# Optimization experiments

Measured on AMD Instinct MI355X. Metric: run time of the kernel, lower is better.

## Reference

```python
import jax, jax.numpy as jnp
import numpy as np

N = 50000      # nodes
E = 800000     # edges
G = 512        # graphs
IN = 544; HID = 64; H = 4; OUT = 2
EPS = 1e-5

def setup_inputs():
    key = jax.random.key(0)
    ks = jax.random.split(key, 16)
    x = jax.random.normal(ks[0], (N, IN), jnp.float32)
    edge_index = jax.random.randint(ks[1], (2, E), 0, N, jnp.int64)
    batch = jnp.sort(jax.random.randint(ks[2], (N,), 0, G, jnp.int64))
    s = lambda k, shp, fan: jax.random.normal(k, shp, jnp.float32) / np.sqrt(fan)
    return {
        'x': x, 'edge_index': edge_index, 'batch': batch,
        'ln_g': jnp.ones((32,), jnp.float32), 'ln_b': jnp.zeros((32,), jnp.float32),
        'bn1_g': jnp.ones((512,), jnp.float32), 'bn1_b': jnp.zeros((512,), jnp.float32),
        'Wc': s(ks[3], (16, 512), 512), 'bc': jnp.zeros((16,), jnp.float32),
        'bn2_g': jnp.ones((48,), jnp.float32), 'bn2_b': jnp.zeros((48,), jnp.float32),
        'Wp': s(ks[4], (HID, 48), 48), 'bp': jnp.zeros((HID,), jnp.float32),
        'Wg': s(ks[5], (H * HID, HID), HID),
        'att_src': s(ks[6], (H, HID), HID), 'att_dst': s(ks[7], (H, HID), HID),
        'bg': jnp.zeros((H * HID,), jnp.float32),
        'bn3_g': jnp.ones((H * HID,), jnp.float32), 'bn3_b': jnp.zeros((H * HID,), jnp.float32),
        'W1': s(ks[8], (HID, H * HID), H * HID), 'b1': jnp.zeros((HID,), jnp.float32),
        'W2': s(ks[9], (OUT, HID), HID), 'b2': jnp.zeros((OUT,), jnp.float32),
    }

def _batchnorm(x, g, b):
    mu = jnp.mean(x, axis=0)
    var = jnp.var(x, axis=0)
    return (x - mu) * jax.lax.rsqrt(var + EPS) * g + b

def _forward(x, ln_g, ln_b, bn1_g, bn1_b, Wc, bc, bn2_g, bn2_b, Wp, bp,
             Wg, att_src, att_dst, bg, bn3_g, bn3_b, W1, b1, W2, b2,
             edge_index, batch):
    # feature split + norms
    x_cnn = _batchnorm(x[:, :512], bn1_g, bn1_b)
    f = x[:, 512:]
    mu = jnp.mean(f, axis=-1, keepdims=True)
    var = jnp.var(f, axis=-1, keepdims=True)
    f = (f - mu) * jax.lax.rsqrt(var + EPS) * ln_g + ln_b
    x_cnn = x_cnn @ Wc.T + bc                      # [N,16]
    z = jnp.concatenate([x_cnn, f], axis=1)        # [N,48]
    z = _batchnorm(z, bn2_g, bn2_b)
    z = jax.nn.relu(z @ Wp.T + bp)                 # [N,HID] (dropout=eval identity)
    # GATConv (concat=True, negative_slope=0.2)
    h = (z @ Wg.T).reshape(N, H, HID)              # [N,H,C]
    a_src = jnp.sum(h * att_src, axis=-1)          # [N,H]
    a_dst = jnp.sum(h * att_dst, axis=-1)          # [N,H]
    src, dst = edge_index[0], edge_index[1]
    e = jax.nn.leaky_relu(a_src[src] + a_dst[dst], 0.2)   # [E,H]
    m = jax.ops.segment_max(e, dst, num_segments=N)
    m = jnp.where(jnp.isfinite(m), m, 0.0)
    ex = jnp.exp(e - m[dst])
    s = jax.ops.segment_sum(ex, dst, num_segments=N)
    alpha = ex / jnp.maximum(s, 1e-16)[dst]               # [E,H]
    out = jax.ops.segment_sum(alpha[:, :, None] * h[src], dst, num_segments=N)
    out = out.reshape(N, H * HID) + bg
    # BatchNorm + ELU + mean pool + MLP head
    out = jax.nn.elu(_batchnorm(out, bn3_g, bn3_b))
    cnt = jax.ops.segment_sum(jnp.ones((N,), out.dtype), batch, num_segments=G)
    pooled = jax.ops.segment_sum(out, batch, num_segments=G) / jnp.maximum(cnt, 1.0)[:, None]
    hmlp = jax.nn.relu(pooled @ W1.T + b1)
    return hmlp @ W2.T + b2                        # [G,OUT]

def reference(x, edge_index, batch, ln_g, ln_b, bn1_g, bn1_b, Wc, bc, bn2_g, bn2_b,
              Wp, bp, Wg, att_src, att_dst, bg, bn3_g, bn3_b, W1, b1, W2, b2):
    return _forward(x, ln_g, ln_b, bn1_g, bn1_b, Wc, bc, bn2_g, bn2_b, Wp, bp,
                    Wg, att_src, att_dst, bg, bn3_g, bn3_b, W1, b1, W2, b2,
                    edge_index, batch)
```

## Files before the change

### kernel.cpp

```cpp
#include <hip/hip_runtime.h>

static constexpr int N_   = 50000;
static constexpr int E_   = 800000;
static constexpr int G_   = 512;
static constexpr int IN_  = 544;
static constexpr float EPS_ = 1e-5f;

static constexpr int BN1C = 32;
static constexpr int BN3C = 16;
static constexpr int BN2C = 8;
static constexpr size_t OFF_BN1C   = 0;
static constexpr size_t OFF_BN2C   = 131072;
static constexpr size_t OFF_BN3C   = 134144;
static constexpr size_t OFF_COUNT  = 166912;
static constexpr size_t OFF_CUR    = 366912;
static constexpr size_t ZERO_BYTES = 566912;
static constexpr size_t OFF_OFFS   = 566912;
static constexpr size_t OFF_WC2    = 766912;
static constexpr size_t OFF_C2     = 799680;
static constexpr size_t OFF_WP2    = 799744;
static constexpr size_t OFF_CP     = 812032;
static constexpr size_t OFF_WGT    = 812288;
static constexpr size_t OFF_PART   = 877824;
static constexpr size_t OFF_ASRC   = 878080;
static constexpr size_t OFF_ADST   = 1678080;
static constexpr size_t OFF_SRCS   = 2478080;
static constexpr size_t OFF_Z      = 5678080;
static constexpr size_t OFF_H      = 15278080;
static constexpr size_t OFF_OUTP   = 40878080;

#define DEV static __device__ __forceinline__

DEV float lrelu(float v) { return v > 0.f ? v : 0.2f * v; }
DEV unsigned short f2bf(float f) {
    unsigned u = __float_as_uint(f);
    return (unsigned short)((u + 0x7fffu + ((u >> 16) & 1u)) >> 16);
}

__global__ __launch_bounds__(256) void k_bn1_hist(
        const float* __restrict__ x, float* __restrict__ bn1c,
        const int* __restrict__ ei, int* __restrict__ count) {
    __shared__ float4 ta[256];
    __shared__ float4 tb[256];
    int t = threadIdx.x;
    int cq = t & 127, rsub = t >> 7;
    int c4 = cq << 2;
    float4 a = make_float4(0.f, 0.f, 0.f, 0.f);
    float4 b = make_float4(0.f, 0.f, 0.f, 0.f);
    for (int r = blockIdx.x * 2 + rsub; r < N_; r += gridDim.x * 2) {
        float4 v = *(const float4*)(x + (size_t)r * IN_ + c4);
        a.x += v.x; a.y += v.y; a.z += v.z; a.w += v.w;
        b.x += v.x * v.x; b.y += v.y * v.y; b.z += v.z * v.z; b.w += v.w * v.w;
    }
    ta[t] = a; tb[t] = b;
    __syncthreads();
    if (t < 128) {
        float4 sa = ta[t], sb = tb[t];
        float4 xa = ta[128 + t], xb = tb[128 + t];
        sa.x += xa.x; sa.y += xa.y; sa.z += xa.z; sa.w += xa.w;
        sb.x += xb.x; sb.y += xb.y; sb.z += xb.z; sb.w += xb.w;
        float* dst = bn1c + (size_t)(blockIdx.x & (BN1C - 1)) * 1024;
        int c = t << 2;
        atomicAdd(&dst[c + 0], sa.x); atomicAdd(&dst[c + 1], sa.y);
        atomicAdd(&dst[c + 2], sa.z); atomicAdd(&dst[c + 3], sa.w);
        atomicAdd(&dst[512 + c + 0], sb.x); atomicAdd(&dst[512 + c + 1], sb.y);
        atomicAdd(&dst[512 + c + 2], sb.z); atomicAdd(&dst[512 + c + 3], sb.w);
    }
    for (int k = blockIdx.x * 256 + t; k < E_; k += gridDim.x * 256)
        atomicAdd(&count[ei[E_ + k]], 1);
}

__global__ __launch_bounds__(512) void k_fold1(
        const float* __restrict__ bn1c,
        const float* __restrict__ g, const float* __restrict__ b,
        const float* __restrict__ Wc, const float* __restrict__ bc,
        float* __restrict__ Wc2t, float* __restrict__ c2) {
    __shared__ float c2s[16];
    int j = threadIdx.x;
    if (j < 16) c2s[j] = 0.f;
    float sum = 0.f, sq = 0.f;
    for (int c = 0; c < BN1C; c++) {
        sum += bn1c[c * 1024 + j];
        sq  += bn1c[c * 1024 + 512 + j];
    }
    float mu  = sum / (float)N_;
    float var = sq / (float)N_ - mu * mu;
    float s   = g[j] * rsqrtf(var + EPS_);
    float tj  = b[j] - mu * s;
    __syncthreads();
    for (int i = 0; i < 16; i++) {
        float wv = Wc[i * 512 + j];
        Wc2t[i * 512 + j] = wv * s;
        float p = tj * wv;
        for (int m = 1; m < 64; m <<= 1) p += __shfl_xor(p, m);
        if ((j & 63) == 0) atomicAdd(&c2s[i], p);
    }
    __syncthreads();
    if (j < 16) c2[j] = c2s[j] + bc[j];
}

static constexpr int WSTRIDE = 516;
__global__ __launch_bounds__(512) void k_z(
        const float* __restrict__ x, const float* __restrict__ Wc2tg,
        const float* __restrict__ c2g, const float* __restrict__ lng,
        const float* __restrict__ lnb, float* __restrict__ z,
        float* __restrict__ bn2c) {
    __shared__ float wc2[16 * WSTRIDE];
    __shared__ float c2s[16];
    __shared__ float bsum[48];
    __shared__ float bsq[48];
    int t = threadIdx.x;
    for (int q = t; q < 8192; q += 512) {
        int row = q >> 9, col = q & 511;
        wc2[row * WSTRIDE + col] = Wc2tg[q];
    }
    if (t < 16) c2s[t] = c2g[t];
    if (t < 48) { bsum[t] = 0.f; bsq[t] = 0.f; }
    __syncthreads();
    int pr = t >> 3, i = t & 7;
    int n0 = blockIdx.x * 128 + pr * 2;
    int n1 = n0 + 1;
    bool v0 = n0 < N_, v1 = n1 < N_;
    const float4* xr0 = (const float4*)(x + (size_t)(v0 ? n0 : N_ - 1) * IN_);
    const float4* xr1 = (const float4*)(x + (size_t)(v1 ? n1 : N_ - 1) * IN_);
    const float4* w0 = (const float4*)(wc2 + i * WSTRIDE);
    const float4* w1 = (const float4*)(wc2 + (i + 8) * WSTRIDE);
    float a00 = c2s[i], a01 = c2s[i + 8];
    float a10 = a00, a11 = a01;
    for (int u = 0; u < 128; u++) {
        float4 xa = xr0[u], xb = xr1[u];
        float4 p = w0[u], q4 = w1[u];
        a00 += xa.x * p.x + xa.y * p.y + xa.z * p.z + xa.w * p.w;
        a01 += xa.x * q4.x + xa.y * q4.y + xa.z * q4.z + xa.w * q4.w;
        a10 += xb.x * p.x + xb.y * p.y + xb.z * p.z + xb.w * p.w;
        a11 += xb.x * q4.x + xb.y * q4.y + xb.z * q4.z + xb.w * q4.w;
    }
    float va[4], vb[4];
    float sm0 = 0.f, sq0 = 0.f, sm1 = 0.f, sq1 = 0.f;
#pragma unroll
    for (int jj = 0; jj < 4; jj++) {
        va[jj] = x[(size_t)(v0 ? n0 : N_ - 1) * IN_ + 512 + i + 8 * jj];
        vb[jj] = x[(size_t)(v1 ? n1 : N_ - 1) * IN_ + 512 + i + 8 * jj];
        sm0 += va[jj]; sq0 += va[jj] * va[jj];
        sm1 += vb[jj]; sq1 += vb[jj] * vb[jj];
    }
    for (int m = 1; m < 8; m <<= 1) {
        sm0 += __shfl_xor(sm0, m); sq0 += __shfl_xor(sq0, m);
        sm1 += __shfl_xor(sm1, m); sq1 += __shfl_xor(sq1, m);
    }
    float mu0 = sm0 * (1.f / 32.f), rs0 = rsqrtf(sq0 * (1.f / 32.f) - mu0 * mu0 + EPS_);
    float mu1 = sm1 * (1.f / 32.f), rs1 = rsqrtf(sq1 * (1.f / 32.f) - mu1 * mu1 + EPS_);
    float outa[6], outb[6];
    outa[0] = a00; outa[1] = a01; outb[0] = a10; outb[1] = a11;
#pragma unroll
    for (int jj = 0; jj < 4; jj++) {
        int c = i + 8 * jj;
        float gg = lng[c], bb = lnb[c];
        outa[2 + jj] = (va[jj] - mu0) * rs0 * gg + bb;
        outb[2 + jj] = (vb[jj] - mu1) * rs1 * gg + bb;
    }
    int cols[6] = { i, i + 8, 16 + i, 24 + i, 32 + i, 40 + i };
    if (v0) {
#pragma unroll
        for (int k = 0; k < 6; k++) z[n0 * 48 + cols[k]] = outa[k];
    }
    if (v1) {
#pragma unroll
        for (int k = 0; k < 6; k++) z[n1 * 48 + cols[k]] = outb[k];
    }
    float s6[6], q6[6];
#pragma unroll
    for (int k = 0; k < 6; k++) {
        float pa = v0 ? outa[k] : 0.f;
        float pb = v1 ? outb[k] : 0.f;
        s6[k] = pa + pb; q6[k] = pa * pa + pb * pb;
    }
#pragma unroll
    for (int m = 8; m < 64; m <<= 1) {
#pragma unroll
        for (int k = 0; k < 6; k++) {
            s6[k] += __shfl_xor(s6[k], m);
            q6[k] += __shfl_xor(q6[k], m);
        }
    }
    if ((t & 63) < 8) {
#pragma unroll
        for (int k = 0; k < 6; k++) {
            atomicAdd(&bsum[cols[k]], s6[k]);
            atomicAdd(&bsq[cols[k]],  q6[k]);
        }
    }
    __syncthreads();
    if (t < 48) {
        float* dst = bn2c + (size_t)(blockIdx.x & (BN2C - 1)) * 96;
        atomicAdd(&dst[t],      bsum[t]);
        atomicAdd(&dst[48 + t], bsq[t]);
    }
}

__global__ __launch_bounds__(256) void k_fold2_wgt(
        const float* __restrict__ bn2c,
        const float* __restrict__ g, const float* __restrict__ b,
        const float* __restrict__ Wp, const float* __restrict__ bp,
        float* __restrict__ Wp2, float* __restrict__ cp,
        const float* __restrict__ Wg, float* __restrict__ Wgt) {
    __shared__ float t2[48];
    int t = threadIdx.x;
    if (blockIdx.x > 0) {
        int idx = (blockIdx.x - 1) * 256 + t;
        int c = idx >> 6, k = idx & 63;
        Wgt[k * 256 + c] = Wg[idx];
        return;
    }
    if (t < 48) {
        float sum = 0.f, sq = 0.f;
        for (int c = 0; c < BN2C; c++) {
            sum += bn2c[c * 96 + t];
            sq  += bn2c[c * 96 + 48 + t];
        }
        float mu  = sum / (float)N_;
        float var = sq / (float)N_ - mu * mu;
        float s   = g[t] * rsqrtf(var + EPS_);
        t2[t] = b[t] - mu * s;
        for (int k = 0; k < 64; k++) Wp2[t * 64 + k] = Wp[k * 48 + t] * s;
    }
    __syncthreads();
    if (t < 64) {
        float acc = bp[t];
        for (int j = 0; j < 48; j++) acc += t2[j] * Wp[t * 48 + j];
        cp[t] = acc;
    }
}

__global__ void k_scan1(const int* __restrict__ count, int* __restrict__ offs,
                        int* __restrict__ part) {
    __shared__ int sd[1024];
    int t = threadIdx.x;
    int idx = blockIdx.x * 1024 + t;
    int v = (idx < N_) ? count[idx] : 0;
    sd[t] = v;
    for (int off = 1; off < 1024; off <<= 1) {
        __syncthreads();
        int tmp = (t >= off) ? sd[t - off] : 0;
        __syncthreads();
        sd[t] += tmp;
    }
    if (idx < N_) offs[idx] = sd[t] - v;
    if (t == 1023) part[blockIdx.x] = sd[1023];
}
__global__ void k_scan23(int* __restrict__ offs, const int* __restrict__ part) {
    __shared__ int bs;
    int t = threadIdx.x, b = blockIdx.x;
    if (t < 64) {
        int v = (t < b) ? part[t] : 0;
        for (int m = 1; m < 64; m <<= 1) v += __shfl_xor(v, m);
        if (t == 0) bs = v;
    }
    __syncthreads();
    int idx = b * 1024 + t;
    if (idx < N_) offs[idx] += bs;
}

__global__ void k_scatter(const int* __restrict__ ei, const int* __restrict__ offs,
                          int* __restrict__ cur, int* __restrict__ srcsort) {
    int k = blockIdx.x * 256 + threadIdx.x;
    int src = ei[k], dst = ei[E_ + k];
    int pos = offs[dst] + atomicAdd(&cur[dst], 1);
    srcsort[pos] = src;
}

__global__ __launch_bounds__(512) void k_h2(
        const float* __restrict__ z, const float* __restrict__ Wp2g,
        const float* __restrict__ cpg, const float* __restrict__ Wgtg,
        const float* __restrict__ att_s, const float* __restrict__ att_d,
        ushort4* __restrict__ hbf, float* __restrict__ asrc, float* __restrict__ adst) {
    __shared__ __align__(16) float4 wgh[32 * 64];
    __shared__ __align__(16) float  z1t[128 * 64];
    __shared__ __align__(16) float  wp2[48 * 64];
    __shared__ float  cps[64];
    __shared__ float4 ats[64];
    __shared__ float4 atd[64];
    int t = threadIdx.x;
    int base = blockIdx.x * 128;
    {
        const float4* z4 = (const float4*)(z + (size_t)base * 48);
        float4* zt4 = (float4*)wgh;
        for (int q = t; q < 1536; q += 512) zt4[q] = z4[q];
    }
    for (int q = t; q < 3072; q += 512) wp2[q] = Wp2g[q];
    if (t < 64) {
        cps[t] = cpg[t];
        ats[t] = ((const float4*)att_s)[t];
        atd[t] = ((const float4*)att_d)[t];
    }
    __syncthreads();
    int w = t >> 6, l = t & 63;
    {
        float wpr[48];
#pragma unroll
        for (int j = 0; j < 48; j++) wpr[j] = wp2[j * 64 + l];
        const float* zt = (const float*)wgh;
        for (int p = 0; p < 16; p++) {
            int nd = p * 8 + w;
            float acc = cps[l];
            const float4* zr4 = (const float4*)(zt + nd * 48);
#pragma unroll
            for (int u = 0; u < 12; u++) {
                float4 zv = zr4[u];
                acc += zv.x * wpr[u * 4 + 0] + zv.y * wpr[u * 4 + 1] +
                       zv.z * wpr[u * 4 + 2] + zv.w * wpr[u * 4 + 3];
            }
            z1t[nd * 64 + l] = fmaxf(acc, 0.f);
        }
    }
    const float4* wg4 = (const float4*)Wgtg;
    float4 acc[16];
#pragma unroll
    for (int nd = 0; nd < 16; nd++) acc[nd] = make_float4(0.f, 0.f, 0.f, 0.f);
    for (int half = 0; half < 2; half++) {
        __syncthreads();
        for (int q = t; q < 2048; q += 512) wgh[q] = wg4[half * 2048 + q];
        __syncthreads();
        int kbase = half * 32;
        for (int k4 = 0; k4 < 8; k4++) {
            float4 wv0 = wgh[(k4 * 4 + 0) * 64 + l];
            float4 wv1 = wgh[(k4 * 4 + 1) * 64 + l];
            float4 wv2 = wgh[(k4 * 4 + 2) * 64 + l];
            float4 wv3 = wgh[(k4 * 4 + 3) * 64 + l];
#pragma unroll
            for (int nd = 0; nd < 16; nd++) {
                float4 zv = *(const float4*)&z1t[(w * 16 + nd) * 64 + kbase + k4 * 4];
                acc[nd].x += zv.x * wv0.x + zv.y * wv1.x + zv.z * wv2.x + zv.w * wv3.x;
                acc[nd].y += zv.x * wv0.y + zv.y * wv1.y + zv.z * wv2.y + zv.w * wv3.y;
                acc[nd].z += zv.x * wv0.z + zv.y * wv1.z + zv.z * wv2.z + zv.w * wv3.z;
                acc[nd].w += zv.x * wv0.w + zv.y * wv1.w + zv.z * wv2.w + zv.w * wv3.w;
            }
        }
    }
    float4 as4 = ats[l], ad4 = atd[l];
#pragma unroll
    for (int nd = 0; nd < 16; nd++) {
        int node = base + w * 16 + nd;
        if (node < N_) {
            ushort4 hv;
            hv.x = f2bf(acc[nd].x); hv.y = f2bf(acc[nd].y);
            hv.z = f2bf(acc[nd].z); hv.w = f2bf(acc[nd].w);
            hbf[(size_t)node * 64 + l] = hv;
            float pa = acc[nd].x * as4.x + acc[nd].y * as4.y +
                       acc[nd].z * as4.z + acc[nd].w * as4.w;
            float pb = acc[nd].x * ad4.x + acc[nd].y * ad4.y +
                       acc[nd].z * ad4.z + acc[nd].w * ad4.w;
            for (int m = 1; m < 16; m <<= 1) {
                pa += __shfl_xor(pa, m);
                pb += __shfl_xor(pb, m);
            }
            if ((l & 15) == 0) {
                asrc[node * 4 + (l >> 4)] = pa;
                adst[node * 4 + (l >> 4)] = pb;
            }
        }
    }
}

__global__ __launch_bounds__(256) void k_agg(
        const int* __restrict__ count, const int* __restrict__ offs,
        const int* __restrict__ srcsort, const float* __restrict__ asrc,
        const float* __restrict__ adst, const ushort4* __restrict__ hbf,
        const float* __restrict__ bg, ushort4* __restrict__ outbf) {
    __shared__ int   s_src[4][128];
    __shared__ float s_wf[4][512];
    int w = threadIdx.x >> 6, l = threadIdx.x & 63;
    int dst = blockIdx.x * 4 + w;
    const float4* asrc4 = (const float4*)asrc;
    float4 bgv = ((const float4*)bg)[l];
    int deg = count[dst];
    if (deg == 0) {
        ushort4 o;
        o.x = f2bf(bgv.x); o.y = f2bf(bgv.y); o.z = f2bf(bgv.z); o.w = f2bf(bgv.w);
        outbf[(size_t)dst * 64 + l] = o;
        return;
    }
    int base = offs[dst];
    float4 ad = ((const float4*)adst)[dst];
    const float NEGINF = -__builtin_inff();
    float4 e0 = make_float4(NEGINF, NEGINF, NEGINF, NEGINF);
    float4 e1 = make_float4(NEGINF, NEGINF, NEGINF, NEGINF);
    if (l < deg) {
        int s0 = srcsort[base + l];
        s_src[w][l] = s0;
        float4 a = asrc4[s0];
        e0 = make_float4(lrelu(a.x + ad.x), lrelu(a.y + ad.y),
                         lrelu(a.z + ad.z), lrelu(a.w + ad.w));
    }
    if (l + 64 < deg) {
        int s1 = srcsort[base + l + 64];
        s_src[w][l + 64] = s1;
        float4 a = asrc4[s1];
        e1 = make_float4(lrelu(a.x + ad.x), lrelu(a.y + ad.y),
                         lrelu(a.z + ad.z), lrelu(a.w + ad.w));
    }
    float4 mx = make_float4(fmaxf(e0.x, e1.x), fmaxf(e0.y, e1.y),
                            fmaxf(e0.z, e1.z), fmaxf(e0.w, e1.w));
    for (int j = l + 128; j < deg; j += 64) {
        int s2 = srcsort[base + j];
        float4 a = asrc4[s2];
        mx.x = fmaxf(mx.x, lrelu(a.x + ad.x)); mx.y = fmaxf(mx.y, lrelu(a.y + ad.y));
        mx.z = fmaxf(mx.z, lrelu(a.z + ad.z)); mx.w = fmaxf(mx.w, lrelu(a.w + ad.w));
    }
    for (int m = 1; m < 64; m <<= 1) {
        mx.x = fmaxf(mx.x, __shfl_xor(mx.x, m));
        mx.y = fmaxf(mx.y, __shfl_xor(mx.y, m));
        mx.z = fmaxf(mx.z, __shfl_xor(mx.z, m));
        mx.w = fmaxf(mx.w, __shfl_xor(mx.w, m));
    }
    float4 sv = make_float4(0.f, 0.f, 0.f, 0.f);
    if (l < deg) {
        float4 ex = make_float4(__expf(e0.x - mx.x), __expf(e0.y - mx.y),
                                __expf(e0.z - mx.z), __expf(e0.w - mx.w));
        *(float4*)&s_wf[w][l * 4] = ex;
        sv.x += ex.x; sv.y += ex.y; sv.z += ex.z; sv.w += ex.w;
    }
    if (l + 64 < deg) {
        float4 ex = make_float4(__expf(e1.x - mx.x), __expf(e1.y - mx.y),
                                __expf(e1.z - mx.z), __expf(e1.w - mx.w));
        *(float4*)&s_wf[w][(l + 64) * 4] = ex;
        sv.x += ex.x; sv.y += ex.y; sv.z += ex.z; sv.w += ex.w;
    }
    for (int j = l + 128; j < deg; j += 64) {
        int s2 = srcsort[base + j];
        float4 a = asrc4[s2];
        sv.x += __expf(lrelu(a.x + ad.x) - mx.x);
        sv.y += __expf(lrelu(a.y + ad.y) - mx.y);
        sv.z += __expf(lrelu(a.z + ad.z) - mx.z);
        sv.w += __expf(lrelu(a.w + ad.w) - mx.w);
    }
    for (int m = 1; m < 64; m <<= 1) {
        sv.x += __shfl_xor(sv.x, m); sv.y += __shfl_xor(sv.y, m);
        sv.z += __shfl_xor(sv.z, m); sv.w += __shfl_xor(sv.w, m);
    }
    int hd = l >> 4;
    float mh  = hd == 0 ? mx.x : hd == 1 ? mx.y : hd == 2 ? mx.z : mx.w;
    float sh  = hd == 0 ? sv.x : hd == 1 ? sv.y : hd == 2 ? sv.z : sv.w;
    float adh = hd == 0 ? ad.x : hd == 1 ? ad.y : hd == 2 ? ad.z : ad.w;
    float inv = 1.f / fmaxf(sh, 1e-16f);
    float4 accv = make_float4(0.f, 0.f, 0.f, 0.f);
    const uint2* h2p = (const uint2*)hbf;
    int dcap = deg < 128 ? deg : 128;
#pragma unroll 2
    for (int j = 0; j < dcap; j++) {
        int src = s_src[w][j];
        float wgt = s_wf[w][j * 4 + hd] * inv;
        uint2 u = h2p[(size_t)src * 64 + l];
        accv.x += wgt * __uint_as_float(u.x << 16);
        accv.y += wgt * __uint_as_float(u.x & 0xffff0000u);
        accv.z += wgt * __uint_as_float(u.y << 16);
        accv.w += wgt * __uint_as_float(u.y & 0xffff0000u);
    }
    for (int j = 128; j < deg; j++) {
        int src = srcsort[base + j];
        float4 a = asrc4[src];
        float ah = hd == 0 ? a.x : hd == 1 ? a.y : hd == 2 ? a.z : a.w;
        float wgt = __expf(lrelu(ah + adh) - mh) * inv;
        uint2 u = h2p[(size_t)src * 64 + l];
        accv.x += wgt * __uint_as_float(u.x << 16);
        accv.y += wgt * __uint_as_float(u.x & 0xffff0000u);
        accv.z += wgt * __uint_as_float(u.y << 16);
        accv.w += wgt * __uint_as_float(u.y & 0xffff0000u);
    }
    ushort4 o;
    o.x = f2bf(accv.x + bgv.x); o.y = f2bf(accv.y + bgv.y);
    o.z = f2bf(accv.z + bgv.z); o.w = f2bf(accv.w + bgv.w);
    outbf[(size_t)dst * 64 + l] = o;
}

__global__ __launch_bounds__(256) void k_bn3_stats(
        const uint2* __restrict__ op2, float* __restrict__ bn3c) {
    __shared__ float4 ta[256];
    __shared__ float4 tb[256];
    int t = threadIdx.x;
    int cq = t & 63, rsub = t >> 6;
    float4 a = make_float4(0.f, 0.f, 0.f, 0.f);
    float4 b = make_float4(0.f, 0.f, 0.f, 0.f);
    for (int r = blockIdx.x * 4 + rsub; r < N_; r += gridDim.x * 4) {
        uint2 u = op2[(size_t)r * 64 + cq];
        float x0 = __uint_as_float(u.x << 16);
        float x1 = __uint_as_float(u.x & 0xffff0000u);
        float x2 = __uint_as_float(u.y << 16);
        float x3 = __uint_as_float(u.y & 0xffff0000u);
        a.x += x0; a.y += x1; a.z += x2; a.w += x3;
        b.x += x0 * x0; b.y += x1 * x1; b.z += x2 * x2; b.w += x3 * x3;
    }
    ta[t] = a; tb[t] = b;
    __syncthreads();
    if (t < 64) {
        float4 sa = ta[t], sb = tb[t];
#pragma unroll
        for (int r = 1; r < 4; r++) {
            float4 xa = ta[r * 64 + t], xb = tb[r * 64 + t];
            sa.x += xa.x; sa.y += xa.y; sa.z += xa.z; sa.w += xa.w;
            sb.x += xb.x; sb.y += xb.y; sb.z += xb.z; sb.w += xb.w;
        }
        float* dst = bn3c + (size_t)(blockIdx.x & (BN3C - 1)) * 512;
        int c = t << 2;
        atomicAdd(&dst[c + 0], sa.x); atomicAdd(&dst[c + 1], sa.y);
        atomicAdd(&dst[c + 2], sa.z); atomicAdd(&dst[c + 3], sa.w);
        atomicAdd(&dst[256 + c + 0], sb.x); atomicAdd(&dst[256 + c + 1], sb.y);
        atomicAdd(&dst[256 + c + 2], sb.z); atomicAdd(&dst[256 + c + 3], sb.w);
    }
}

__global__ __launch_bounds__(256) void k_pool_mlp(
        const uint2* __restrict__ op2, const int* __restrict__ batch,
        const float* __restrict__ bn3c,
        const float* __restrict__ bn3g, const float* __restrict__ bn3b,
        const float* __restrict__ W1, const float* __restrict__ b1,
        const float* __restrict__ W2, const float* __restrict__ b2,
        float* __restrict__ out) {
    __shared__ float4 tile[256];
    __shared__ float  pl[256];
    __shared__ float  hm[64];
    __shared__ float  s3[256];
    __shared__ float  q3[256];
    int g = blockIdx.x;
    int t = threadIdx.x;
    int cq = t & 63, rsub = t >> 6;
    int c4 = cq << 2;
    {
        float s = 0.f, q = 0.f;
        for (int c = 0; c < BN3C; c++) {
            s += bn3c[c * 512 + t];
            q += bn3c[c * 512 + 256 + t];
        }
        s3[t] = s; q3[t] = q;
    }
    int lo = 0, hi = N_;
    while (lo < hi) { int mid = (lo + hi) >> 1; if (batch[mid] < g) lo = mid + 1; else hi = mid; }
    int start = lo;
    hi = N_;
    while (lo < hi) { int mid = (lo + hi) >> 1; if (batch[mid] < g + 1) lo = mid + 1; else hi = mid; }
    int end = lo;
    __syncthreads();
    float scv[4], shv[4];
#pragma unroll
    for (int k = 0; k < 4; k++) {
        int c = c4 + k;
        float mu  = s3[c] / (float)N_;
        float var = q3[c] / (float)N_ - mu * mu;
        float s   = bn3g[c] * rsqrtf(var + EPS_);
        scv[k] = s; shv[k] = bn3b[c] - mu * s;
    }
    float4 acc = make_float4(0.f, 0.f, 0.f, 0.f);
    for (int n = start + rsub; n < end; n += 4) {
        uint2 u = op2[(size_t)n * 64 + cq];
        float e0 = __uint_as_float(u.x << 16)          * scv[0] + shv[0];
        float e1 = __uint_as_float(u.x & 0xffff0000u)  * scv[1] + shv[1];
        float e2 = __uint_as_float(u.y << 16)          * scv[2] + shv[2];
        float e3 = __uint_as_float(u.y & 0xffff0000u)  * scv[3] + shv[3];
        acc.x += (e0 > 0.f) ? e0 : expm1f(e0);
        acc.y += (e1 > 0.f) ? e1 : expm1f(e1);
        acc.z += (e2 > 0.f) ? e2 : expm1f(e2);
        acc.w += (e3 > 0.f) ? e3 : expm1f(e3);
    }
    tile[t] = acc;
    __syncthreads();
    if (t < 64) {
        float4 s = tile[t];
#pragma unroll
        for (int r = 1; r < 4; r++) {
            float4 xv = tile[r * 64 + t];
            s.x += xv.x; s.y += xv.y; s.z += xv.z; s.w += xv.w;
        }
        float icn = 1.f / fmaxf((float)(end - start), 1.f);
        ((float4*)pl)[t] = make_float4(s.x * icn, s.y * icn, s.z * icn, s.w * icn);
    }
    __syncthreads();
    {
        int j = t >> 2, part = t & 3;
        const float* w1r = W1 + j * 256 + part * 64;
        const float* plr = pl + part * 64;
        float a = 0.f;
#pragma unroll
        for (int c = 0; c < 64; c++) a += w1r[c] * plr[c];
        a += __shfl_xor(a, 1);
        a += __shfl_xor(a, 2);
        if (part == 0) hm[j] = fmaxf(a + b1[j], 0.f);
    }
    __syncthreads();
    if (t < 128) {
        int j = t >> 6, k = t & 63;
        float p = W2[j * 64 + k] * hm[k];
        for (int m = 1; m < 64; m <<= 1) p += __shfl_xor(p, m);
        if (k == 0) out[g * 2 + j] = p + b2[j];
    }
}

extern "C" void kernel_launch(void* const* d_in, const int* in_sizes, int n_in,
                              void* d_out, int out_size, void* d_ws, size_t ws_size,
                              hipStream_t stream) {
    const float* x    = (const float*)d_in[0];
    const int*   ei   = (const int*)d_in[1];
    const int*   batch= (const int*)d_in[2];
    const float* lng  = (const float*)d_in[3];
    const float* lnb  = (const float*)d_in[4];
    const float* bn1g = (const float*)d_in[5];
    const float* bn1b = (const float*)d_in[6];
    const float* Wc   = (const float*)d_in[7];
    const float* bc   = (const float*)d_in[8];
    const float* bn2g = (const float*)d_in[9];
    const float* bn2b = (const float*)d_in[10];
    const float* Wp   = (const float*)d_in[11];
    const float* bp   = (const float*)d_in[12];
    const float* Wg   = (const float*)d_in[13];
    const float* atts = (const float*)d_in[14];
    const float* attd = (const float*)d_in[15];
    const float* bg   = (const float*)d_in[16];
    const float* bn3g = (const float*)d_in[17];
    const float* bn3b = (const float*)d_in[18];
    const float* W1   = (const float*)d_in[19];
    const float* b1   = (const float*)d_in[20];
    const float* W2   = (const float*)d_in[21];
    const float* b2   = (const float*)d_in[22];
    float* out = (float*)d_out;

    char* w8 = (char*)d_ws;
    float* bn1c   = (float*)(w8 + OFF_BN1C);
    float* bn2c   = (float*)(w8 + OFF_BN2C);
    float* bn3c   = (float*)(w8 + OFF_BN3C);
    int*   count  = (int*)(w8 + OFF_COUNT);
    int*   cur    = (int*)(w8 + OFF_CUR);
    int*   offs   = (int*)(w8 + OFF_OFFS);
    int*   part   = (int*)(w8 + OFF_PART);
    float* Wc2t   = (float*)(w8 + OFF_WC2);
    float* c2     = (float*)(w8 + OFF_C2);
    float* Wp2    = (float*)(w8 + OFF_WP2);
    float* cp     = (float*)(w8 + OFF_CP);
    float* Wgt    = (float*)(w8 + OFF_WGT);
    float* asrc   = (float*)(w8 + OFF_ASRC);
    float* adst   = (float*)(w8 + OFF_ADST);
    int*   srcs   = (int*)(w8 + OFF_SRCS);
    float* z      = (float*)(w8 + OFF_Z);
    ushort4* hbf  = (ushort4*)(w8 + OFF_H);
    ushort4* outp = (ushort4*)(w8 + OFF_OUTP);

    hipMemsetAsync(d_ws, 0, ZERO_BYTES, stream);

    k_bn1_hist<<<2048, 256, 0, stream>>>(x, bn1c, ei, count);
    k_fold1<<<1, 512, 0, stream>>>(bn1c, bn1g, bn1b, Wc, bc, Wc2t, c2);
    k_z<<<(N_ + 127) / 128, 512, 0, stream>>>(x, Wc2t, c2, lng, lnb, z, bn2c);
    const int SCANB = (N_ + 1023) / 1024;
    k_scan1<<<SCANB, 1024, 0, stream>>>(count, offs, part);
    k_scan23<<<SCANB, 1024, 0, stream>>>(offs, part);
    k_fold2_wgt<<<65, 256, 0, stream>>>(bn2c, bn2g, bn2b, Wp, bp, Wp2, cp, Wg, Wgt);
    k_scatter<<<E_ / 256, 256, 0, stream>>>(ei, offs, cur, srcs);
    k_h2<<<(N_ + 127) / 128, 512, 0, stream>>>(z, Wp2, cp, Wgt, atts, attd, hbf, asrc, adst);
    k_agg<<<N_ / 4, 256, 0, stream>>>(count, offs, srcs, asrc, adst, hbf, bg, outp);
    k_bn3_stats<<<1024, 256, 0, stream>>>((const uint2*)outp, bn3c);
    k_pool_mlp<<<G_, 256, 0, stream>>>((const uint2*)outp, batch, bn3c,
                                       bn3g, bn3b, W1, b1, W2, b2, out);
}
```

Measured before the change: 551.2 us.

## Replace global-atomic CSR build with two-pass LDS radix sort by destination

Swaps the global-atomic degree histogram, three-kernel scan and atomic scatter for a two-pass radix sort keyed on the destination node. The first pass bins edges by the high bits of dst using per-block LDS histograms, a column scan and a scatter. The second pass sorts each bucket by the low 8 bits in LDS and writes count, offsets and the sorted source array. This targets contended global atomics and random scattered writes, at the cost of more kernel launches and an extra round trip of intermediate sorted arrays through memory.

```diff
diff --git a/kernel.cpp b/kernel.cpp
--- a/kernel.cpp
+++ b/kernel.cpp
@@ -5,6 +5,7 @@
 static constexpr int G_   = 512;
 static constexpr int IN_  = 544;
 static constexpr float EPS_ = 1e-5f;
+static constexpr int NBLK = 782;
 
 static constexpr int BN1C = 32;
 static constexpr int BN3C = 16;
@@ -12,22 +13,25 @@
 static constexpr size_t OFF_BN1C   = 0;
 static constexpr size_t OFF_BN2C   = 131072;
 static constexpr size_t OFF_BN3C   = 134144;
+static constexpr size_t ZERO_BYTES = 166912;
 static constexpr size_t OFF_COUNT  = 166912;
-static constexpr size_t OFF_CUR    = 366912;
-static constexpr size_t ZERO_BYTES = 566912;
-static constexpr size_t OFF_OFFS   = 566912;
-static constexpr size_t OFF_WC2    = 766912;
-static constexpr size_t OFF_C2     = 799680;
-static constexpr size_t OFF_WP2    = 799744;
-static constexpr size_t OFF_CP     = 812032;
-static constexpr size_t OFF_WGT    = 812288;
-static constexpr size_t OFF_PART   = 877824;
-static constexpr size_t OFF_ASRC   = 878080;
-static constexpr size_t OFF_ADST   = 1678080;
-static constexpr size_t OFF_SRCS   = 2478080;
-static constexpr size_t OFF_Z      = 5678080;
-static constexpr size_t OFF_H      = 15278080;
-static constexpr size_t OFF_OUTP   = 40878080;
+static constexpr size_t OFF_OFFS   = 366912;
+static constexpr size_t OFF_BH     = 566912;
+static constexpr size_t OFF_BTOT   = 1367680;
+static constexpr size_t OFF_BBASE  = 1368704;
+static constexpr size_t OFF_SORTD  = 1369856;
+static constexpr size_t OFF_SORTS  = 2969856;
+static constexpr size_t OFF_SRCS   = 6169856;
+static constexpr size_t OFF_WC2    = 9369856;
+static constexpr size_t OFF_C2     = 9402624;
+static constexpr size_t OFF_WP2    = 9402880;
+static constexpr size_t OFF_CP     = 9415168;
+static constexpr size_t OFF_WGT    = 9415424;
+static constexpr size_t OFF_ASRC   = 9480960;
+static constexpr size_t OFF_ADST   = 10280960;
+static constexpr size_t OFF_Z      = 11080960;
+static constexpr size_t OFF_H      = 20680960;
+static constexpr size_t OFF_OUTP   = 46280960;
 
 #define DEV static __device__ __forceinline__
 
@@ -37,9 +41,8 @@
     return (unsigned short)((u + 0x7fffu + ((u >> 16) & 1u)) >> 16);
 }
 
-__global__ __launch_bounds__(256) void k_bn1_hist(
-        const float* __restrict__ x, float* __restrict__ bn1c,
-        const int* __restrict__ ei, int* __restrict__ count) {
+__global__ __launch_bounds__(256) void k_bn1(
+        const float* __restrict__ x, float* __restrict__ bn1c) {
     __shared__ float4 ta[256];
     __shared__ float4 tb[256];
     int t = threadIdx.x;
@@ -66,8 +69,123 @@
         atomicAdd(&dst[512 + c + 0], sb.x); atomicAdd(&dst[512 + c + 1], sb.y);
         atomicAdd(&dst[512 + c + 2], sb.z); atomicAdd(&dst[512 + c + 3], sb.w);
     }
-    for (int k = blockIdx.x * 256 + t; k < E_; k += gridDim.x * 256)
-        atomicAdd(&count[ei[E_ + k]], 1);
+}
+
+__global__ __launch_bounds__(256) void k_rhist(
+        const int* __restrict__ ei, int* __restrict__ blockhist) {
+    __shared__ int hist[256];
+    int t = threadIdx.x;
+    hist[t] = 0;
+    __syncthreads();
+    int base = blockIdx.x * 1024;
+#pragma unroll
+    for (int k = 0; k < 4; k++) {
+        int i = base + k * 256 + t;
+        if (i < E_) atomicAdd(&hist[ei[E_ + i] >> 8], 1);
+    }
+    __syncthreads();
+    blockhist[blockIdx.x * 256 + t] = hist[t];
+}
+
+__global__ __launch_bounds__(256) void k_rscan(
+        int* __restrict__ blockhist, int* __restrict__ btot) {
+    __shared__ int a[256];
+    int b = blockIdx.x, t = threadIdx.x;
+    int v[4]; int s = 0;
+#pragma unroll
+    for (int k = 0; k < 4; k++) {
+        int j = t * 4 + k;
+        v[k] = (j < NBLK) ? blockhist[j * 256 + b] : 0;
+        s += v[k];
+    }
+    a[t] = s;
+    for (int off = 1; off < 256; off <<= 1) {
+        __syncthreads();
+        int tmp = (t >= off) ? a[t - off] : 0;
+        __syncthreads();
+        a[t] += tmp;
+    }
+    __syncthreads();
+    int run = a[t] - s;
+#pragma unroll
+    for (int k = 0; k < 4; k++) {
+        int j = t * 4 + k;
+        if (j < NBLK) { blockhist[j * 256 + b] = run; run += v[k]; }
+    }
+    if (t == 255) btot[b] = a[255];
+}
+
+__global__ __launch_bounds__(256) void k_rbase(
+        const int* __restrict__ btot, int* __restrict__ bbase) {
+    __shared__ int a[256];
+    int t = threadIdx.x;
+    int v = btot[t];
+    a[t] = v;
+    for (int off = 1; off < 256; off <<= 1) {
+        __syncthreads();
+        int tmp = (t >= off) ? a[t - off] : 0;
+        __syncthreads();
+        a[t] += tmp;
+    }
+    __syncthreads();
+    bbase[t] = a[t] - v;
+    if (t == 255) bbase[256] = a[255];
+}
+
+__global__ __launch_bounds__(256) void k_rscatter(
+        const int* __restrict__ ei, const int* __restrict__ blockhist,
+        const int* __restrict__ bbase, unsigned short* __restrict__ sortd,
+        int* __restrict__ sorts) {
+    __shared__ int cursor[256];
+    int t = threadIdx.x;
+    cursor[t] = bbase[t] + blockhist[blockIdx.x * 256 + t];
+    __syncthreads();
+    int base = blockIdx.x * 1024;
+#pragma unroll
+    for (int k = 0; k < 4; k++) {
+        int i = base + k * 256 + t;
+        if (i < E_) {
+            int d = ei[E_ + i], s = ei[i];
+            int pos = atomicAdd(&cursor[d >> 8], 1);
+            sortd[pos] = (unsigned short)d;
+            sorts[pos] = s;
+        }
+    }
+}
+
+__global__ __launch_bounds__(256) void k_rsort2(
+        const unsigned short* __restrict__ sortd, const int* __restrict__ sorts,
+        const int* __restrict__ bbase, int* __restrict__ count,
+        int* __restrict__ offs, int* __restrict__ srcsort) {
+    __shared__ int hist[256];
+    __shared__ int pref[256];
+    __shared__ int cursor[256];
+    int b = blockIdx.x, t = threadIdx.x;
+    int base = bbase[b], endp = bbase[b + 1];
+    hist[t] = 0;
+    __syncthreads();
+    for (int i = base + t; i < endp; i += 256)
+        atomicAdd(&hist[sortd[i] & 255], 1);
+    __syncthreads();
+    int hv = hist[t];
+    pref[t] = hv;
+    for (int off = 1; off < 256; off <<= 1) {
+        __syncthreads();
+        int tmp = (t >= off) ? pref[t - off] : 0;
+        __syncthreads();
+        pref[t] += tmp;
+    }
+    __syncthreads();
+    int ex = pref[t] - hv;
+    int idx = (b << 8) + t;
+    if (idx < N_) { count[idx] = hv; offs[idx] = base + ex; }
+    cursor[t] = ex;
+    __syncthreads();
+    for (int i = base + t; i < endp; i += 256) {
+        int d = sortd[i], s = sorts[i];
+        int pos = base + atomicAdd(&cursor[d & 255], 1);
+        srcsort[pos] = s;
+    }
 }
 
 __global__ __launch_bounds__(512) void k_fold1(
@@ -230,43 +348,6 @@
         for (int j = 0; j < 48; j++) acc += t2[j] * Wp[t * 48 + j];
         cp[t] = acc;
     }
-}
-
-__global__ void k_scan1(const int* __restrict__ count, int* __restrict__ offs,
-                        int* __restrict__ part) {
-    __shared__ int sd[1024];
-    int t = threadIdx.x;
-    int idx = blockIdx.x * 1024 + t;
-    int v = (idx < N_) ? count[idx] : 0;
-    sd[t] = v;
-    for (int off = 1; off < 1024; off <<= 1) {
-        __syncthreads();
-        int tmp = (t >= off) ? sd[t - off] : 0;
-        __syncthreads();
-        sd[t] += tmp;
-    }
-    if (idx < N_) offs[idx] = sd[t] - v;
-    if (t == 1023) part[blockIdx.x] = sd[1023];
-}
-__global__ void k_scan23(int* __restrict__ offs, const int* __restrict__ part) {
-    __shared__ int bs;
-    int t = threadIdx.x, b = blockIdx.x;
-    if (t < 64) {
-        int v = (t < b) ? part[t] : 0;
-        for (int m = 1; m < 64; m <<= 1) v += __shfl_xor(v, m);
-        if (t == 0) bs = v;
-    }
-    __syncthreads();
-    int idx = b * 1024 + t;
-    if (idx < N_) offs[idx] += bs;
-}
-
-__global__ void k_scatter(const int* __restrict__ ei, const int* __restrict__ offs,
-                          int* __restrict__ cur, int* __restrict__ srcsort) {
-    int k = blockIdx.x * 256 + threadIdx.x;
-    int src = ei[k], dst = ei[E_ + k];
-    int pos = offs[dst] + atomicAdd(&cur[dst], 1);
-    srcsort[pos] = src;
 }
 
 __global__ __launch_bounds__(512) void k_h2(
@@ -627,9 +708,13 @@
     float* bn2c   = (float*)(w8 + OFF_BN2C);
     float* bn3c   = (float*)(w8 + OFF_BN3C);
     int*   count  = (int*)(w8 + OFF_COUNT);
-    int*   cur    = (int*)(w8 + OFF_CUR);
     int*   offs   = (int*)(w8 + OFF_OFFS);
-    int*   part   = (int*)(w8 + OFF_PART);
+    int*   bh     = (int*)(w8 + OFF_BH);
+    int*   btot   = (int*)(w8 + OFF_BTOT);
+    int*   bbase  = (int*)(w8 + OFF_BBASE);
+    unsigned short* sortd = (unsigned short*)(w8 + OFF_SORTD);
+    int*   sorts  = (int*)(w8 + OFF_SORTS);
+    int*   srcs   = (int*)(w8 + OFF_SRCS);
     float* Wc2t   = (float*)(w8 + OFF_WC2);
     float* c2     = (float*)(w8 + OFF_C2);
     float* Wp2    = (float*)(w8 + OFF_WP2);
@@ -637,21 +722,21 @@
     float* Wgt    = (float*)(w8 + OFF_WGT);
     float* asrc   = (float*)(w8 + OFF_ASRC);
     float* adst   = (float*)(w8 + OFF_ADST);
-    int*   srcs   = (int*)(w8 + OFF_SRCS);
     float* z      = (float*)(w8 + OFF_Z);
     ushort4* hbf  = (ushort4*)(w8 + OFF_H);
     ushort4* outp = (ushort4*)(w8 + OFF_OUTP);
 
     hipMemsetAsync(d_ws, 0, ZERO_BYTES, stream);
 
-    k_bn1_hist<<<2048, 256, 0, stream>>>(x, bn1c, ei, count);
+    k_bn1<<<2048, 256, 0, stream>>>(x, bn1c);
+    k_rhist<<<NBLK, 256, 0, stream>>>(ei, bh);
     k_fold1<<<1, 512, 0, stream>>>(bn1c, bn1g, bn1b, Wc, bc, Wc2t, c2);
+    k_rscan<<<256, 256, 0, stream>>>(bh, btot);
     k_z<<<(N_ + 127) / 128, 512, 0, stream>>>(x, Wc2t, c2, lng, lnb, z, bn2c);
-    const int SCANB = (N_ + 1023) / 1024;
-    k_scan1<<<SCANB, 1024, 0, stream>>>(count, offs, part);
-    k_scan23<<<SCANB, 1024, 0, stream>>>(offs, part);
+    k_rbase<<<1, 256, 0, stream>>>(btot, bbase);
+    k_rscatter<<<NBLK, 256, 0, stream>>>(ei, bh, bbase, sortd, sorts);
     k_fold2_wgt<<<65, 256, 0, stream>>>(bn2c, bn2g, bn2b, Wp, bp, Wp2, cp, Wg, Wgt);
-    k_scatter<<<E_ / 256, 256, 0, stream>>>(ei, offs, cur, srcs);
+    k_rsort2<<<196, 256, 0, stream>>>(sortd, sorts, bbase, count, offs, srcs);
     k_h2<<<(N_ + 127) / 128, 512, 0, stream>>>(z, Wp2, cp, Wgt, atts, attd, hbf, asrc, adst);
     k_agg<<<N_ / 4, 256, 0, stream>>>(count, offs, srcs, asrc, adst, hbf, bg, outp);
     k_bn3_stats<<<1024, 256, 0, stream>>>((const uint2*)outp, bn3c);
```

Result: faster. 519.4 us (-5.8%).
